# Optimization experiments

Measured on AMD Instinct MI355X. Metric: run time of the kernel, lower is better.

Reference implementation:

```python
import jax, jax.numpy as jnp
import numpy as np

N, E, B, IN, H = 20000, 50000, 1024, 32, 64

def setup_inputs() -> dict:
    key = jax.random.key(0)
    ks = jax.random.split(key, 32)
    d = {}
    d["x"] = jax.random.normal(ks[0], (N, IN), jnp.float32)
    d["edge_index"] = jax.random.randint(ks[1], (2, E), 0, N)
    d["edge_attr"] = jax.random.uniform(ks[2], (E, 6), dtype=jnp.float32)
    d["batch"] = jnp.sort(jax.random.randint(ks[3], (N,), 0, B))
    d["t"] = jax.random.uniform(ks[4], (B, 1), dtype=jnp.float32)
    d["p"] = jax.random.uniform(ks[5], (B, 1), dtype=jnp.float32)
    d["num_graphs"] = B
    def lin(k, fan_in, shape):
        return jax.random.normal(k, shape, jnp.float32) * (1.0 / np.sqrt(fan_in))
    # lin0: IN -> H
    d["W0"] = lin(ks[6], IN, (IN, H)); d["b0"] = jnp.zeros((H,), jnp.float32)
    # edge MLP: 6 -> 64 -> H*H
    d["We1"] = lin(ks[7], 6, (6, 64)); d["be1"] = jnp.zeros((64,), jnp.float32)
    d["We2"] = lin(ks[8], 64, (64, H * H)); d["be2"] = jnp.zeros((H * H,), jnp.float32)
    # NNConv root weight + bias
    d["Wroot"] = lin(ks[9], H, (H, H)); d["bconv"] = jnp.zeros((H,), jnp.float32)
    # GRU (input H, hidden H), torch layout [3H, *] gate order r,z,n
    d["gru_wih"] = lin(ks[10], H, (3 * H, H)); d["gru_whh"] = lin(ks[11], H, (3 * H, H))
    d["gru_bih"] = jnp.zeros((3 * H,), jnp.float32); d["gru_bhh"] = jnp.zeros((3 * H,), jnp.float32)
    # Set2Set LSTM (input 2H, hidden H), torch layout [4H, *] gate order i,f,g,o
    d["l_wih"] = lin(ks[12], 2 * H, (4 * H, 2 * H)); d["l_whh"] = lin(ks[13], H, (4 * H, H))
    d["l_bih"] = jnp.zeros((4 * H,), jnp.float32); d["l_bhh"] = jnp.zeros((4 * H,), jnp.float32)
    # readout MLP
    d["W1"] = lin(ks[14], 2 * H + 2, (2 * H + 2, H)); d["b1"] = jnp.zeros((H,), jnp.float32)
    d["W2"] = lin(ks[15], H, (H, 64)); d["b2"] = jnp.zeros((64,), jnp.float32)
    d["W3"] = lin(ks[16], 64, (64, 1)); d["b3"] = jnp.zeros((1,), jnp.float32)
    return d


def reference(x, edge_attr, t, p, W0, b0, We1, be1, We2, be2, Wroot, bconv,
              gru_wih, gru_whh, gru_bih, gru_bhh, l_wih, l_whh, l_bih, l_bhh,
              W1, b1, W2, b2, W3, b3, edge_index, batch, num_graphs):
    n_nodes = x.shape[0]
    hdim = W0.shape[1]
    src, dst = edge_index[0], edge_index[1]

    out = jax.nn.relu(x @ W0 + b0)            # [N,H]
    h = out

    # edge MLP -> per-edge weight matrices [E,H,H] (edge_attr is loop-invariant)
    ew = (jax.nn.relu(edge_attr @ We1 + be1) @ We2 + be2).reshape(-1, hdim, hdim)

    for _ in range(4):
        # NNConv: gather source features, per-edge matmul, scatter-add to targets
        msg = jnp.einsum('eh,eho->eo', out[src], ew)                 # [E,H]
        agg = jax.ops.segment_sum(msg, dst, num_segments=n_nodes)    # [N,H]
        m = jax.nn.relu(agg + out @ Wroot + bconv)
        # GRU step (single timestep)
        gi = m @ gru_wih.T + gru_bih
        gh = h @ gru_whh.T + gru_bhh
        ir, iz, inn = jnp.split(gi, 3, axis=-1)
        hr, hz, hn = jnp.split(gh, 3, axis=-1)
        r = jax.nn.sigmoid(ir + hr)
        z = jax.nn.sigmoid(iz + hz)
        nn_ = jnp.tanh(inn + r * hn)
        h = (1.0 - z) * nn_ + z * h
        out = h

    # Set2Set pooling, 3 processing steps
    qh = jnp.zeros((num_graphs, hdim), x.dtype)
    qc = jnp.zeros((num_graphs, hdim), x.dtype)
    q_star = jnp.zeros((num_graphs, 2 * hdim), x.dtype)
    for _ in range(3):
        g = q_star @ l_wih.T + l_bih + qh @ l_whh.T + l_bhh
        gi_, gf_, gg_, go_ = jnp.split(g, 4, axis=-1)
        qc = jax.nn.sigmoid(gf_) * qc + jax.nn.sigmoid(gi_) * jnp.tanh(gg_)
        qh = jax.nn.sigmoid(go_) * jnp.tanh(qc)
        q = qh                                                        # [B,H]
        e = jnp.sum(out * q[batch], axis=-1, keepdims=True)          # [N,1]
        emax = jax.ops.segment_max(e, batch, num_segments=num_graphs)
        a = jnp.exp(e - emax[batch])
        asum = jax.ops.segment_sum(a, batch, num_segments=num_graphs)
        a = a / asum[batch]                                           # segment softmax
        r_ = jax.ops.segment_sum(a * out, batch, num_segments=num_graphs)
        q_star = jnp.concatenate([q, r_], axis=-1)

    feat = jnp.concatenate([q_star, t, p], axis=-1)                   # [B,2H+2]
    y = jax.nn.relu(feat @ W1 + b1)
    y = jax.nn.relu(y @ W2 + b2)
    y = y @ W3 + b3
    return y.reshape(-1)
```

## Files before the change

### kernel.cpp

```cpp
#include <hip/hip_runtime.h>
#include <math.h>

#define N_NODES 20000
#define N_EDGES 50000
#define NB      1024
#define IND     32
#define HDIM    64

typedef __attribute__((ext_vector_type(8))) short bf16x8;
typedef __attribute__((ext_vector_type(4))) float f32x4;

static inline size_t align_up(size_t x, size_t a) { return (x + a - 1) & ~(a - 1); }

__device__ __forceinline__ float sigmoidf_(float x) {
    return 1.0f / (1.0f + __expf(-x));
}
__device__ __forceinline__ float tanhf_(float x) {
    float xc = fminf(fmaxf(x, -15.0f), 15.0f);
    float e = __expf(2.0f * xc);
    return (e - 1.0f) / (e + 1.0f);
}
__device__ __forceinline__ unsigned pk2(float p0, float p1) {
    unsigned u0 = __float_as_uint(p0) + 0x8000u;
    unsigned u1 = __float_as_uint(p1) + 0x8000u;
    return __builtin_amdgcn_perm(u1, u0, 0x07060302u);
}
__device__ __forceinline__ unsigned bf1(float v) {
    return (__float_as_uint(v) + 0x8000u) >> 16;
}

__global__ void k_prep(const float* __restrict__ We2, const float* __restrict__ be2,
                       short* __restrict__ We2b,
                       const float* __restrict__ Wroot, const float* __restrict__ gwhh,
                       const float* __restrict__ gwih,
                       short* __restrict__ WB1h, short* __restrict__ WB1l,
                       short* __restrict__ WB2h, short* __restrict__ WB2l,
                       const float* __restrict__ lwih, const float* __restrict__ lwhh,
                       float* __restrict__ lwihP, float* __restrict__ lwhhP,
                       const int* __restrict__ batch, int* __restrict__ offs) {
    int bid = blockIdx.x, tid = threadIdx.x;
    if (bid < 1040) {
        int idx = bid * 256 + tid;
        int s = idx >> 12;
        int col = idx & 4095;
        int k = col >> 6, o = col & 63;
        float val = (s < 64) ? We2[k * 4096 + s * 64 + o] : be2[k * 64 + o];
        int dst = s * 4096 + (((o >> 4) * 128 + (k >> 5) * 64 + ((k >> 3) & 3) * 16 + (o & 15)) << 3) + (k & 7);
        We2b[dst] = (short)bf1(val);
    } else if (bid < 1152) {
        int idx = (bid - 1040) * 256 + tid;
        if (idx < 28672) {
            bool b1 = idx < 16384;
            int li = b1 ? idx : idx - 16384;
            int j = li & 7, lane = (li >> 3) & 63, c = (li >> 9) & 1, otile = li >> 10;
            int k = c * 32 + (lane >> 4) * 8 + j;
            int o = otile * 16 + (lane & 15);
            float val;
            if (b1) val = (o < 64) ? Wroot[k * 64 + o] : gwhh[(o - 64) * 64 + k];
            else    val = gwih[o * 64 + k];
            unsigned hs = bf1(val);
            float lo = val - __uint_as_float(hs << 16);
            unsigned ls = bf1(lo);
            if (b1) { WB1h[li] = (short)hs; WB1l[li] = (short)ls; }
            else    { WB2h[li] = (short)hs; WB2l[li] = (short)ls; }
        }
    } else if (bid < 1280) {
        int idx = (bid - 1152) * 256 + tid;
        int g = idx & 3, j = (idx >> 2) & 63, i = idx >> 8;
        lwihP[idx] = lwih[(g * 64 + j) * 128 + i];
    } else if (bid < 1344) {
        int idx = (bid - 1280) * 256 + tid;
        int g = idx & 3, j = (idx >> 2) & 63, i = idx >> 8;
        lwhhP[idx] = lwhh[(g * 64 + j) * 64 + i];
    } else {
        int i = (bid - 1344) * 256 + tid;
        if (i <= NB) {
            int lo = 0, hi = N_NODES;
            while (lo < hi) { int mid = (lo + hi) >> 1; if (batch[mid] < i) lo = mid + 1; else hi = mid; }
            offs[i] = lo;
        }
    }
}

__global__ void k_count(const int* __restrict__ ei, int* __restrict__ deg) {
    int e = blockIdx.x * 256 + threadIdx.x;
    if (e < N_EDGES) atomicAdd(&deg[ei[N_EDGES + e]], 1);
}

__global__ void k_scan(const int* __restrict__ deg, int* __restrict__ rowptr, int* __restrict__ cursor) {
    __shared__ int s_w[16];
    int t = threadIdx.x;
    int base = t * 20;
    int v[20]; int s = 0;
#pragma unroll
    for (int i = 0; i < 20; ++i) {
        int idx = base + i;
        v[i] = (idx < N_NODES) ? deg[idx] : 0;
        s += v[i];
    }
    int lane = t & 63, w = t >> 6;
    int inc = s;
#pragma unroll
    for (int off = 1; off < 64; off <<= 1) {
        int o = __shfl_up(inc, off);
        if (lane >= off) inc += o;
    }
    if (lane == 63) s_w[w] = inc;
    __syncthreads();
    if (w == 0 && lane < 16) {
        int x = s_w[lane];
        int xs = x;
#pragma unroll
        for (int off = 1; off < 16; off <<= 1) {
            int o = __shfl_up(xs, off);
            if (lane >= off) xs += o;
        }
        s_w[lane] = xs - x;
    }
    __syncthreads();
    int run = s_w[w] + (inc - s);
#pragma unroll
    for (int i = 0; i < 20; ++i) {
        int idx = base + i;
        if (idx < N_NODES) { rowptr[idx] = run; cursor[idx] = run; }
        else if (idx == N_NODES) rowptr[idx] = run;
        run += v[i];
    }
}

__global__ void k_fill(const int* __restrict__ ei, int* __restrict__ cursor, int* __restrict__ perm) {
    int e = blockIdx.x * 256 + threadIdx.x;
    if (e < N_EDGES) {
        int pos = atomicAdd(&cursor[ei[N_EDGES + e]], 1);
        perm[pos] = e;
    }
}

__global__ void k_init_feat(const float* __restrict__ x, const float* __restrict__ W0,
                            const float* __restrict__ b0, float* __restrict__ hbuf,
                            const float* __restrict__ ea, const float* __restrict__ We1,
                            const float* __restrict__ be1, float* __restrict__ re) {
    int bid = blockIdx.x;
    int tid = threadIdx.x;
    int w = tid >> 6, j = tid & 63;
    if (bid < 5000) {
        int n = bid * 4 + w;
        float acc = b0[j];
        const float* xr = x + n * IND;
#pragma unroll
        for (int i = 0; i < IND; ++i) acc = fmaf(xr[i], W0[i * 64 + j], acc);
        hbuf[n * 64 + j] = fmaxf(acc, 0.0f);
    } else {
        int e = (bid - 5000) * 4 + w;
        if (e >= N_EDGES) return;
        float acc = be1[j];
        const float* er = ea + e * 6;
#pragma unroll
        for (int i = 0; i < 6; ++i) acc = fmaf(er[i], We1[i * 64 + j], acc);
        re[e * 64 + j] = fmaxf(acc, 0.0f);
    }
}

__launch_bounds__(256, 3)
__global__ void k_msg_mfma(const float* __restrict__ hbuf, const float* __restrict__ reb,
                           const short* __restrict__ We2b, const int* __restrict__ ei,
                           float* __restrict__ msg) {
    __shared__ float s_v[64][64];
    int tid = threadIdx.x;
    int eb = blockIdx.x * 64;
    int lane = tid & 63;
    int w = tid >> 6;
    int l15 = lane & 15, lhi = lane >> 4;

    {
        int se = tid >> 2;
        int sh = tid & 3;
        int ge = eb + se;
        const float* rowp = (ge < N_EDGES) ? (hbuf + (size_t)ei[ge] * 64) : (const float*)0;
#pragma unroll
        for (int rr4 = 0; rr4 < 4; ++rr4) {
            int hb = rr4 * 16 + sh * 4;
            float4 vv = rowp ? *(const float4*)(rowp + hb) : make_float4(0.f, 0.f, 0.f, 0.f);
            s_v[hb + 0][se] = vv.x; s_v[hb + 1][se] = vv.y;
            s_v[hb + 2][se] = vv.z; s_v[hb + 3][se] = vv.w;
        }
    }

    union U { int4 i4; bf16x8 v; };
    U a_re[4][2];
#pragma unroll
    for (int m = 0; m < 4; ++m) {
        int ge = eb + m * 16 + l15;
        if (ge < N_EDGES) {
            const float* rp = reb + (size_t)ge * 64 + lhi * 8;
            float4 x0 = *(const float4*)(rp);
            float4 x1 = *(const float4*)(rp + 4);
            float4 y0 = *(const float4*)(rp + 32);
            float4 y1 = *(const float4*)(rp + 36);
            a_re[m][0].i4 = make_int4(pk2(x0.x, x0.y), pk2(x0.z, x0.w), pk2(x1.x, x1.y), pk2(x1.z, x1.w));
            a_re[m][1].i4 = make_int4(pk2(y0.x, y0.y), pk2(y0.z, y0.w), pk2(y1.x, y1.y), pk2(y1.z, y1.w));
        } else {
            a_re[m][0].i4 = make_int4(0, 0, 0, 0);
            a_re[m][1].i4 = make_int4(0, 0, 0, 0);
        }
    }

    const int4* bp0 = (const int4*)We2b + (w * 128 + lane);
    const int4* bp1 = bp0 + 64;
    int4 Sc0[4], Sc1[4];
#pragma unroll
    for (int j = 0; j < 4; ++j) {
        Sc0[j] = bp0[j * 512];
        Sc1[j] = bp1[j * 512];
    }

    __syncthreads();

    const f32x4 zero4 = {0.f, 0.f, 0.f, 0.f};
    f32x4 macc[4];
#pragma unroll
    for (int m = 0; m < 4; ++m) macc[m] = zero4;

    float4 vv[4], vn[4];
#pragma unroll
    for (int m = 0; m < 4; ++m) vv[m] = *(const float4*)&s_v[0][m * 16 + lhi * 4];

    for (int g = 0; g < 16; ++g) {
#pragma unroll
        for (int j = 0; j < 4; ++j) {
            int s = g * 4 + j;
            int snext = (s < 63) ? (s + 1) : 63;
#pragma unroll
            for (int m = 0; m < 4; ++m)
                vn[m] = *(const float4*)&s_v[snext][m * 16 + lhi * 4];
            U bb0, bb1; bb0.i4 = Sc0[j]; bb1.i4 = Sc1[j];
#pragma unroll
            for (int m = 0; m < 4; ++m) {
                f32x4 t = __builtin_amdgcn_mfma_f32_16x16x32_bf16(a_re[m][0].v, bb0.v, zero4, 0, 0, 0);
                t = __builtin_amdgcn_mfma_f32_16x16x32_bf16(a_re[m][1].v, bb1.v, t, 0, 0, 0);
                macc[m][0] = fmaf(vv[m].x, t[0], macc[m][0]);
                macc[m][1] = fmaf(vv[m].y, t[1], macc[m][1]);
                macc[m][2] = fmaf(vv[m].z, t[2], macc[m][2]);
                macc[m][3] = fmaf(vv[m].w, t[3], macc[m][3]);
            }
            int sload = (s + 4 <= 64) ? (s + 4) : 64;
            Sc0[j] = bp0[sload * 512];
            Sc1[j] = bp1[sload * 512];
#pragma unroll
            for (int m = 0; m < 4; ++m) vv[m] = vn[m];
        }
    }

    {
        U bb0, bb1; bb0.i4 = Sc0[0]; bb1.i4 = Sc1[0];
#pragma unroll
        for (int m = 0; m < 4; ++m) {
            int e = m * 16 + l15;
            U a0, a1;
            a0.i4 = make_int4(
                pk2(s_v[lhi * 8 + 0][e], s_v[lhi * 8 + 1][e]),
                pk2(s_v[lhi * 8 + 2][e], s_v[lhi * 8 + 3][e]),
                pk2(s_v[lhi * 8 + 4][e], s_v[lhi * 8 + 5][e]),
                pk2(s_v[lhi * 8 + 6][e], s_v[lhi * 8 + 7][e]));
            a1.i4 = make_int4(
                pk2(s_v[32 + lhi * 8 + 0][e], s_v[32 + lhi * 8 + 1][e]),
                pk2(s_v[32 + lhi * 8 + 2][e], s_v[32 + lhi * 8 + 3][e]),
                pk2(s_v[32 + lhi * 8 + 4][e], s_v[32 + lhi * 8 + 5][e]),
                pk2(s_v[32 + lhi * 8 + 6][e], s_v[32 + lhi * 8 + 7][e]));
            macc[m] = __builtin_amdgcn_mfma_f32_16x16x32_bf16(a0.v, bb0.v, macc[m], 0, 0, 0);
            macc[m] = __builtin_amdgcn_mfma_f32_16x16x32_bf16(a1.v, bb1.v, macc[m], 0, 0, 0);
        }
    }
    int o = w * 16 + l15;
#pragma unroll
    for (int m = 0; m < 4; ++m) {
#pragma unroll
        for (int r = 0; r < 4; ++r) {
            int el = m * 16 + lhi * 4 + r;
            int ge = eb + el;
            if (ge < N_EDGES) msg[(size_t)ge * 64 + o] = macc[m][r];
        }
    }
}

__launch_bounds__(256, 4)
__global__ void k_node_update(float* __restrict__ hbuf, const float* __restrict__ msg,
                              const int* __restrict__ rowptr, const int* __restrict__ perm,
                              const short* __restrict__ WB1h, const short* __restrict__ WB1l,
                              const short* __restrict__ WB2h, const short* __restrict__ WB2l,
                              const float* __restrict__ bconv, const float* __restrict__ bih,
                              const float* __restrict__ bhh) {
    __shared__ short s_hh[32][72];
    __shared__ short s_hl[32][72];
    __shared__ short s_mh[32][72];
    __shared__ short s_ml[32][72];
    __shared__ float s_agg[32][68];
    int tid = threadIdx.x;
    int nbase = blockIdx.x * 32;
    int lane = tid & 63, w = tid >> 6;
    int l15 = lane & 15, lhi = lane >> 4;

    {
        int nt = tid >> 3, q = tid & 7;
        int n = nbase + nt;
#pragma unroll
        for (int c4 = 0; c4 < 2; ++c4) {
            int col = q * 8 + c4 * 4;
            float4 v = *(const float4*)&hbuf[(size_t)n * 64 + col];
            unsigned h01 = pk2(v.x, v.y), h23 = pk2(v.z, v.w);
            float f0 = __uint_as_float(h01 << 16);
            float f1 = __uint_as_float(h01 & 0xffff0000u);
            float f2 = __uint_as_float(h23 << 16);
            float f3 = __uint_as_float(h23 & 0xffff0000u);
            unsigned l01 = pk2(v.x - f0, v.y - f1), l23 = pk2(v.z - f2, v.w - f3);
            *(unsigned*)&s_hh[nt][col]     = h01;
            *(unsigned*)&s_hh[nt][col + 2] = h23;
            *(unsigned*)&s_hl[nt][col]     = l01;
            *(unsigned*)&s_hl[nt][col + 2] = l23;
        }
        float4 aggv[2];
#pragma unroll
        for (int c4 = 0; c4 < 2; ++c4)
            aggv[c4] = *(const float4*)&bconv[q * 8 + c4 * 4];
        int rs = rowptr[n], rend = rowptr[n + 1];
        for (int qq = rs; qq < rend; ++qq) {
            const float* mrow = msg + (size_t)perm[qq] * 64 + q * 8;
#pragma unroll
            for (int c4 = 0; c4 < 2; ++c4) {
                float4 mv = *(const float4*)&mrow[c4 * 4];
                aggv[c4].x += mv.x; aggv[c4].y += mv.y;
                aggv[c4].z += mv.z; aggv[c4].w += mv.w;
            }
        }
#pragma unroll
        for (int c4 = 0; c4 < 2; ++c4)
            *(float4*)&s_agg[nt][q * 8 + c4 * 4] = aggv[c4];
    }
    __syncthreads();

    union U { int4 i4; bf16x8 v; };
    U ah[2][2], al[2][2];
#pragma unroll
    for (int m = 0; m < 2; ++m)
#pragma unroll
        for (int c = 0; c < 2; ++c) {
            ah[m][c].i4 = *(const int4*)&s_hh[m * 16 + l15][c * 32 + lhi * 8];
            al[m][c].i4 = *(const int4*)&s_hl[m * 16 + l15][c * 32 + lhi * 8];
        }

    const int4* B1h = (const int4*)WB1h;
    const int4* B1l = (const int4*)WB1l;
    const int4* B2h = (const int4*)WB2h;
    const int4* B2l = (const int4*)WB2l;

    f32x4 C0[2], G[3][2], I[3][2];

    {
        int ot = w;
        U bh0, bh1, bl0, bl1;
        bh0.i4 = B1h[(ot * 2 + 0) * 64 + lane];
        bh1.i4 = B1h[(ot * 2 + 1) * 64 + lane];
        bl0.i4 = B1l[(ot * 2 + 0) * 64 + lane];
        bl1.i4 = B1l[(ot * 2 + 1) * 64 + lane];
#pragma unroll
        for (int m = 0; m < 2; ++m) {
            f32x4 c;
#pragma unroll
            for (int r = 0; r < 4; ++r) c[r] = s_agg[m * 16 + lhi * 4 + r][w * 16 + l15];
            c = __builtin_amdgcn_mfma_f32_16x16x32_bf16(ah[m][0].v, bh0.v, c, 0, 0, 0);
            c = __builtin_amdgcn_mfma_f32_16x16x32_bf16(ah[m][1].v, bh1.v, c, 0, 0, 0);
            c = __builtin_amdgcn_mfma_f32_16x16x32_bf16(al[m][0].v, bh0.v, c, 0, 0, 0);
            c = __builtin_amdgcn_mfma_f32_16x16x32_bf16(al[m][1].v, bh1.v, c, 0, 0, 0);
            c = __builtin_amdgcn_mfma_f32_16x16x32_bf16(ah[m][0].v, bl0.v, c, 0, 0, 0);
            c = __builtin_amdgcn_mfma_f32_16x16x32_bf16(ah[m][1].v, bl1.v, c, 0, 0, 0);
            C0[m] = c;
        }
    }
#pragma unroll
    for (int m = 0; m < 2; ++m)
#pragma unroll
        for (int r = 0; r < 4; ++r) {
            float mv = fmaxf(C0[m][r], 0.0f);
            int row = m * 16 + lhi * 4 + r, col = w * 16 + l15;
            unsigned hs = bf1(mv);
            float lof = mv - __uint_as_float(hs << 16);
            s_mh[row][col] = (short)hs;
            s_ml[row][col] = (short)bf1(lof);
        }
#pragma unroll
    for (int p = 1; p < 4; ++p) {
        int ot = p * 4 + w;
        U bh0, bh1, bl0, bl1;
        bh0.i4 = B1h[(ot * 2 + 0) * 64 + lane];
        bh1.i4 = B1h[(ot * 2 + 1) * 64 + lane];
        bl0.i4 = B1l[(ot * 2 + 0) * 64 + lane];
        bl1.i4 = B1l[(ot * 2 + 1) * 64 + lane];
        float bv = bhh[(p - 1) * 64 + w * 16 + l15];
#pragma unroll
        for (int m = 0; m < 2; ++m) {
            f32x4 c = {bv, bv, bv, bv};
            c = __builtin_amdgcn_mfma_f32_16x16x32_bf16(ah[m][0].v, bh0.v, c, 0, 0, 0);
            c = __builtin_amdgcn_mfma_f32_16x16x32_bf16(ah[m][1].v, bh1.v, c, 0, 0, 0);
            c = __builtin_amdgcn_mfma_f32_16x16x32_bf16(al[m][0].v, bh0.v, c, 0, 0, 0);
            c = __builtin_amdgcn_mfma_f32_16x16x32_bf16(al[m][1].v, bh1.v, c, 0, 0, 0);
            c = __builtin_amdgcn_mfma_f32_16x16x32_bf16(ah[m][0].v, bl0.v, c, 0, 0, 0);
            c = __builtin_amdgcn_mfma_f32_16x16x32_bf16(ah[m][1].v, bl1.v, c, 0, 0, 0);
            G[p - 1][m] = c;
        }
    }
    __syncthreads();
    U mh[2][2], ml[2][2];
#pragma unroll
    for (int m = 0; m < 2; ++m)
#pragma unroll
        for (int c = 0; c < 2; ++c) {
            mh[m][c].i4 = *(const int4*)&s_mh[m * 16 + l15][c * 32 + lhi * 8];
            ml[m][c].i4 = *(const int4*)&s_ml[m * 16 + l15][c * 32 + lhi * 8];
        }
#pragma unroll
    for (int p = 0; p < 3; ++p) {
        int ot = p * 4 + w;
        U bh0, bh1, bl0, bl1;
        bh0.i4 = B2h[(ot * 2 + 0) * 64 + lane];
        bh1.i4 = B2h[(ot * 2 + 1) * 64 + lane];
        bl0.i4 = B2l[(ot * 2 + 0) * 64 + lane];
        bl1.i4 = B2l[(ot * 2 + 1) * 64 + lane];
        float bv = bih[p * 64 + w * 16 + l15];
#pragma unroll
        for (int m = 0; m < 2; ++m) {
            f32x4 c = {bv, bv, bv, bv};
            c = __builtin_amdgcn_mfma_f32_16x16x32_bf16(mh[m][0].v, bh0.v, c, 0, 0, 0);
            c = __builtin_amdgcn_mfma_f32_16x16x32_bf16(mh[m][1].v, bh1.v, c, 0, 0, 0);
            c = __builtin_amdgcn_mfma_f32_16x16x32_bf16(ml[m][0].v, bh0.v, c, 0, 0, 0);
            c = __builtin_amdgcn_mfma_f32_16x16x32_bf16(ml[m][1].v, bh1.v, c, 0, 0, 0);
            c = __builtin_amdgcn_mfma_f32_16x16x32_bf16(mh[m][0].v, bl0.v, c, 0, 0, 0);
            c = __builtin_amdgcn_mfma_f32_16x16x32_bf16(mh[m][1].v, bl1.v, c, 0, 0, 0);
            I[p][m] = c;
        }
    }
#pragma unroll
    for (int m = 0; m < 2; ++m)
#pragma unroll
        for (int r = 0; r < 4; ++r) {
            int row = m * 16 + lhi * 4 + r;
            int n = nbase + row;
            int col = w * 16 + l15;
            float hold = __uint_as_float(((unsigned)(unsigned short)s_hh[row][col]) << 16)
                       + __uint_as_float(((unsigned)(unsigned short)s_hl[row][col]) << 16);
            float rg = sigmoidf_(I[0][m][r] + G[0][m][r]);
            float z  = sigmoidf_(I[1][m][r] + G[1][m][r]);
            float nn = tanhf_(I[2][m][r] + rg * G[2][m][r]);
            hbuf[(size_t)n * 64 + col] = (1.0f - z) * nn + z * hold;
        }
}

__launch_bounds__(64)
__global__ void k_set2set(const float* __restrict__ hbuf, const int* __restrict__ offs,
                          const float* __restrict__ t, const float* __restrict__ p,
                          const float* __restrict__ lwihP, const float* __restrict__ lwhhP,
                          const float* __restrict__ l_bih, const float* __restrict__ l_bhh,
                          const float* __restrict__ W1, const float* __restrict__ b1,
                          const float* __restrict__ W2, const float* __restrict__ b2,
                          const float* __restrict__ W3, const float* __restrict__ b3,
                          float* __restrict__ y) {
    __shared__ float s_qs[192];
    __shared__ float s_y[64];
    int b = blockIdx.x;
    int j = threadIdx.x;
    int s = offs[b], e = offs[b + 1];
    float qh = 0.f, qc = 0.f, qs0 = 0.f, qs1 = 0.f;
    float bi0 = l_bih[j]       + l_bhh[j];
    float bi1 = l_bih[64 + j]  + l_bhh[64 + j];
    float bi2 = l_bih[128 + j] + l_bhh[128 + j];
    float bi3 = l_bih[192 + j] + l_bhh[192 + j];

    for (int iter = 0; iter < 3; ++iter) {
        s_qs[j] = qs0; s_qs[64 + j] = qs1; s_qs[128 + j] = qh;
        __syncthreads();
        float g0 = bi0, g1 = bi1, g2 = bi2, g3 = bi3;
#pragma unroll 8
        for (int i = 0; i < 128; ++i) {
            float qsv = s_qs[i];
            float4 wv = *(const float4*)&lwihP[(i * 64 + j) * 4];
            g0 = fmaf(qsv, wv.x, g0);
            g1 = fmaf(qsv, wv.y, g1);
            g2 = fmaf(qsv, wv.z, g2);
            g3 = fmaf(qsv, wv.w, g3);
        }
#pragma unroll 8
        for (int i = 0; i < 64; ++i) {
            float qhv = s_qs[128 + i];
            float4 wv = *(const float4*)&lwhhP[(i * 64 + j) * 4];
            g0 = fmaf(qhv, wv.x, g0);
            g1 = fmaf(qhv, wv.y, g1);
            g2 = fmaf(qhv, wv.z, g2);
            g3 = fmaf(qhv, wv.w, g3);
        }
        __syncthreads();
        float ci = sigmoidf_(g0), cf = sigmoidf_(g1);
        float cg = tanhf_(g2),   co = sigmoidf_(g3);
        qc = cf * qc + ci * cg;
        qh = co * tanhf_(qc);
        float qv = qh;
        float mx = -1e30f, l = 0.0f, racc = 0.0f;
        for (int n = s; n < e; ++n) {
            float xv = hbuf[(size_t)n * 64 + j];
            float prod = xv * qv;
#pragma unroll
            for (int off = 32; off > 0; off >>= 1) prod += __shfl_xor(prod, off);
            float mnew = fmaxf(mx, prod);
            float scale = __expf(mx - mnew);
            float wgt = __expf(prod - mnew);
            l = l * scale + wgt;
            racc = racc * scale + wgt * xv;
            mx = mnew;
        }
        float r = (e > s) ? (racc / l) : 0.0f;
        qs0 = qv; qs1 = r;
    }
    s_qs[j] = qs0; s_qs[64 + j] = qs1;
    __syncthreads();
    float acc = b1[j];
#pragma unroll 8
    for (int i = 0; i < 128; ++i) acc = fmaf(s_qs[i], W1[i * 64 + j], acc);
    acc = fmaf(t[b], W1[128 * 64 + j], acc);
    acc = fmaf(p[b], W1[129 * 64 + j], acc);
    acc = fmaxf(acc, 0.0f);
    s_y[j] = acc;
    __syncthreads();
    float acc2 = b2[j];
#pragma unroll 8
    for (int i = 0; i < 64; ++i) acc2 = fmaf(s_y[i], W2[i * 64 + j], acc2);
    acc2 = fmaxf(acc2, 0.0f);
    float part = acc2 * W3[j];
#pragma unroll
    for (int off = 32; off > 0; off >>= 1) part += __shfl_xor(part, off);
    if (j == 0) y[b] = part + b3[0];
}

extern "C" void kernel_launch(void* const* d_in, const int* in_sizes, int n_in,
                              void* d_out, int out_size, void* d_ws, size_t ws_size,
                              hipStream_t stream) {
    const float* x     = (const float*)d_in[0];
    const int*   ei    = (const int*)  d_in[1];
    const float* ea    = (const float*)d_in[2];
    const int*   batch = (const int*)  d_in[3];
    const float* t     = (const float*)d_in[4];
    const float* p     = (const float*)d_in[5];
    const float* W0    = (const float*)d_in[7];
    const float* b0    = (const float*)d_in[8];
    const float* We1   = (const float*)d_in[9];
    const float* be1   = (const float*)d_in[10];
    const float* We2   = (const float*)d_in[11];
    const float* be2   = (const float*)d_in[12];
    const float* Wroot = (const float*)d_in[13];
    const float* bconv = (const float*)d_in[14];
    const float* gwih  = (const float*)d_in[15];
    const float* gwhh  = (const float*)d_in[16];
    const float* gbih  = (const float*)d_in[17];
    const float* gbhh  = (const float*)d_in[18];
    const float* lwih  = (const float*)d_in[19];
    const float* lwhh  = (const float*)d_in[20];
    const float* lbih  = (const float*)d_in[21];
    const float* lbhh  = (const float*)d_in[22];
    const float* W1    = (const float*)d_in[23];
    const float* b1    = (const float*)d_in[24];
    const float* W2    = (const float*)d_in[25];
    const float* b2    = (const float*)d_in[26];
    const float* W3    = (const float*)d_in[27];
    const float* b3    = (const float*)d_in[28];
    float* y = (float*)d_out;

    char* ws = (char*)d_ws;
    size_t off = 0;
    auto alloc = [&](size_t nbytes) {
        void* ptr = (void*)(ws + off);
        off += align_up(nbytes, 256);
        return ptr;
    };
    float* hbuf   = (float*)alloc((size_t)N_NODES * 64 * 4);
    float* reb    = (float*)alloc((size_t)N_EDGES * 64 * 4);
    float* msg    = (float*)alloc((size_t)N_EDGES * 64 * 4);
    short* We2b   = (short*)alloc((size_t)65 * 4096 * 2);
    short* WB1h   = (short*)alloc(16384 * 2);
    short* WB1l   = (short*)alloc(16384 * 2);
    short* WB2h   = (short*)alloc(12288 * 2);
    short* WB2l   = (short*)alloc(12288 * 2);
    float* lwihP  = (float*)alloc(32768 * 4);
    float* lwhhP  = (float*)alloc(16384 * 4);
    int*   offs   = (int*)  alloc((NB + 1) * 4);
    int*   deg    = (int*)  alloc(N_NODES * 4);
    int*   rowptr = (int*)  alloc((N_NODES + 1) * 4);
    int*   cursor = (int*)  alloc(N_NODES * 4);
    int*   perm   = (int*)  alloc(N_EDGES * 4);

    k_prep<<<1349, 256, 0, stream>>>(We2, be2, We2b, Wroot, gwhh, gwih,
                                     WB1h, WB1l, WB2h, WB2l,
                                     lwih, lwhh, lwihP, lwhhP, batch, offs);
    hipMemsetAsync(deg, 0, (size_t)N_NODES * 4, stream);
    k_count<<<(N_EDGES + 255) / 256, 256, 0, stream>>>(ei, deg);
    k_scan<<<1, 1024, 0, stream>>>(deg, rowptr, cursor);
    k_fill<<<(N_EDGES + 255) / 256, 256, 0, stream>>>(ei, cursor, perm);

    k_init_feat<<<17500, 256, 0, stream>>>(x, W0, b0, hbuf, ea, We1, be1, reb);

    for (int it = 0; it < 4; ++it) {
        k_msg_mfma<<<(N_EDGES + 63) / 64, 256, 0, stream>>>(hbuf, reb, We2b, ei, msg);
        k_node_update<<<N_NODES / 32, 256, 0, stream>>>(hbuf, msg, rowptr, perm,
                                                        WB1h, WB1l, WB2h, WB2l,
                                                        bconv, gbih, gbhh);
    }

    k_set2set<<<NB, 64, 0, stream>>>(hbuf, offs, t, p, lwihP, lwhhP, lbih, lbhh,
                                     W1, b1, W2, b2, W3, b3, y);
}
```

Measured before the change: 446.7 us.

## Widen Set2Set blocks to four waves, splitting gate rows and node softmax

The Set2Set kernel now runs 256 threads per graph instead of 64. Each thread computes one LSTM gate pre-activation using transposed weights, and the four waves each take every fourth node in the online softmax. The partial max, sum and accumulator values are then merged in shared memory. This exposes more parallelism for the serial per-graph loop, at the cost of extra barriers and a cross-wave merge step.

```diff
diff --git a/kernel.cpp b/kernel.cpp
--- a/kernel.cpp
+++ b/kernel.cpp
@@ -36,7 +36,7 @@
                        short* __restrict__ WB1h, short* __restrict__ WB1l,
                        short* __restrict__ WB2h, short* __restrict__ WB2l,
                        const float* __restrict__ lwih, const float* __restrict__ lwhh,
-                       float* __restrict__ lwihP, float* __restrict__ lwhhP,
+                       float* __restrict__ lwihT, float* __restrict__ lwhhT,
                        const int* __restrict__ batch, int* __restrict__ offs) {
     int bid = blockIdx.x, tid = threadIdx.x;
     if (bid < 1040) {
@@ -66,12 +66,12 @@
         }
     } else if (bid < 1280) {
         int idx = (bid - 1152) * 256 + tid;
-        int g = idx & 3, j = (idx >> 2) & 63, i = idx >> 8;
-        lwihP[idx] = lwih[(g * 64 + j) * 128 + i];
+        int i = idx >> 8, j = idx & 255;
+        lwihT[idx] = lwih[j * 128 + i];
     } else if (bid < 1344) {
         int idx = (bid - 1280) * 256 + tid;
-        int g = idx & 3, j = (idx >> 2) & 63, i = idx >> 8;
-        lwhhP[idx] = lwhh[(g * 64 + j) * 64 + i];
+        int i = idx >> 8, j = idx & 255;
+        lwhhT[idx] = lwhh[j * 64 + i];
     } else {
         int i = (bid - 1344) * 256 + tid;
         if (i <= NB) {
@@ -454,57 +454,53 @@
         }
 }
 
-__launch_bounds__(64)
+__launch_bounds__(256)
 __global__ void k_set2set(const float* __restrict__ hbuf, const int* __restrict__ offs,
                           const float* __restrict__ t, const float* __restrict__ p,
-                          const float* __restrict__ lwihP, const float* __restrict__ lwhhP,
+                          const float* __restrict__ lwihT, const float* __restrict__ lwhhT,
                           const float* __restrict__ l_bih, const float* __restrict__ l_bhh,
                           const float* __restrict__ W1, const float* __restrict__ b1,
                           const float* __restrict__ W2, const float* __restrict__ b2,
                           const float* __restrict__ W3, const float* __restrict__ b3,
                           float* __restrict__ y) {
     __shared__ float s_qs[192];
+    __shared__ float s_g[256];
+    __shared__ float s_racc[4][64];
+    __shared__ float s_m[4], s_l[4];
     __shared__ float s_y[64];
     int b = blockIdx.x;
-    int j = threadIdx.x;
+    int tid = threadIdx.x;
+    int w = tid >> 6, lane = tid & 63;
     int s = offs[b], e = offs[b + 1];
-    float qh = 0.f, qc = 0.f, qs0 = 0.f, qs1 = 0.f;
-    float bi0 = l_bih[j]       + l_bhh[j];
-    float bi1 = l_bih[64 + j]  + l_bhh[64 + j];
-    float bi2 = l_bih[128 + j] + l_bhh[128 + j];
-    float bi3 = l_bih[192 + j] + l_bhh[192 + j];
+    float bi = l_bih[tid] + l_bhh[tid];
+    float qc = 0.f;
+
+    if (tid < 192) s_qs[tid] = 0.f;
+    __syncthreads();
 
     for (int iter = 0; iter < 3; ++iter) {
-        s_qs[j] = qs0; s_qs[64 + j] = qs1; s_qs[128 + j] = qh;
+        float g = bi;
+#pragma unroll 8
+        for (int i = 0; i < 128; ++i) g = fmaf(s_qs[i], lwihT[i * 256 + tid], g);
+#pragma unroll 8
+        for (int i = 0; i < 64; ++i)  g = fmaf(s_qs[128 + i], lwhhT[i * 256 + tid], g);
+        s_g[tid] = g;
         __syncthreads();
-        float g0 = bi0, g1 = bi1, g2 = bi2, g3 = bi3;
-#pragma unroll 8
-        for (int i = 0; i < 128; ++i) {
-            float qsv = s_qs[i];
-            float4 wv = *(const float4*)&lwihP[(i * 64 + j) * 4];
-            g0 = fmaf(qsv, wv.x, g0);
-            g1 = fmaf(qsv, wv.y, g1);
-            g2 = fmaf(qsv, wv.z, g2);
-            g3 = fmaf(qsv, wv.w, g3);
-        }
-#pragma unroll 8
-        for (int i = 0; i < 64; ++i) {
-            float qhv = s_qs[128 + i];
-            float4 wv = *(const float4*)&lwhhP[(i * 64 + j) * 4];
-            g0 = fmaf(qhv, wv.x, g0);
-            g1 = fmaf(qhv, wv.y, g1);
-            g2 = fmaf(qhv, wv.z, g2);
-            g3 = fmaf(qhv, wv.w, g3);
+        if (w == 0) {
+            float ci = sigmoidf_(s_g[lane]);
+            float cf = sigmoidf_(s_g[64 + lane]);
+            float cg = tanhf_(s_g[128 + lane]);
+            float co = sigmoidf_(s_g[192 + lane]);
+            qc = cf * qc + ci * cg;
+            float qh = co * tanhf_(qc);
+            s_qs[lane] = qh;
+            s_qs[128 + lane] = qh;
         }
         __syncthreads();
-        float ci = sigmoidf_(g0), cf = sigmoidf_(g1);
-        float cg = tanhf_(g2),   co = sigmoidf_(g3);
-        qc = cf * qc + ci * cg;
-        qh = co * tanhf_(qc);
-        float qv = qh;
+        float qv = s_qs[128 + lane];
         float mx = -1e30f, l = 0.0f, racc = 0.0f;
-        for (int n = s; n < e; ++n) {
-            float xv = hbuf[(size_t)n * 64 + j];
+        for (int n = s + w; n < e; n += 4) {
+            float xv = hbuf[(size_t)n * 64 + lane];
             float prod = xv * qv;
 #pragma unroll
             for (int off = 32; off > 0; off >>= 1) prod += __shfl_xor(prod, off);
@@ -515,27 +511,39 @@
             racc = racc * scale + wgt * xv;
             mx = mnew;
         }
-        float r = (e > s) ? (racc / l) : 0.0f;
-        qs0 = qv; qs1 = r;
-    }
-    s_qs[j] = qs0; s_qs[64 + j] = qs1;
-    __syncthreads();
-    float acc = b1[j];
+        s_racc[w][lane] = racc;
+        if (lane == 0) { s_m[w] = mx; s_l[w] = l; }
+        __syncthreads();
+        if (w == 0) {
+            float M = fmaxf(fmaxf(s_m[0], s_m[1]), fmaxf(s_m[2], s_m[3]));
+            float L = 0.f, R = 0.f;
+#pragma unroll
+            for (int ww = 0; ww < 4; ++ww) {
+                float sc = __expf(s_m[ww] - M);
+                L += s_l[ww] * sc;
+                R = fmaf(s_racc[ww][lane], sc, R);
+            }
+            s_qs[64 + lane] = (e > s) ? (R / L) : 0.0f;
+        }
+        __syncthreads();
+    }
+    if (w == 0) {
+        float acc = b1[lane];
 #pragma unroll 8
-    for (int i = 0; i < 128; ++i) acc = fmaf(s_qs[i], W1[i * 64 + j], acc);
-    acc = fmaf(t[b], W1[128 * 64 + j], acc);
-    acc = fmaf(p[b], W1[129 * 64 + j], acc);
-    acc = fmaxf(acc, 0.0f);
-    s_y[j] = acc;
-    __syncthreads();
-    float acc2 = b2[j];
+        for (int i = 0; i < 128; ++i) acc = fmaf(s_qs[i], W1[i * 64 + lane], acc);
+        acc = fmaf(t[b], W1[128 * 64 + lane], acc);
+        acc = fmaf(p[b], W1[129 * 64 + lane], acc);
+        acc = fmaxf(acc, 0.0f);
+        s_y[lane] = acc;
+        float acc2 = b2[lane];
 #pragma unroll 8
-    for (int i = 0; i < 64; ++i) acc2 = fmaf(s_y[i], W2[i * 64 + j], acc2);
-    acc2 = fmaxf(acc2, 0.0f);
-    float part = acc2 * W3[j];
-#pragma unroll
-    for (int off = 32; off > 0; off >>= 1) part += __shfl_xor(part, off);
-    if (j == 0) y[b] = part + b3[0];
+        for (int i = 0; i < 64; ++i) acc2 = fmaf(s_y[i], W2[i * 64 + lane], acc2);
+        acc2 = fmaxf(acc2, 0.0f);
+        float part = acc2 * W3[lane];
+#pragma unroll
+        for (int off = 32; off > 0; off >>= 1) part += __shfl_xor(part, off);
+        if (lane == 0) y[b] = part + b3[0];
+    }
 }
 
 extern "C" void kernel_launch(void* const* d_in, const int* in_sizes, int n_in,
@@ -586,8 +594,8 @@
     short* WB1l   = (short*)alloc(16384 * 2);
     short* WB2h   = (short*)alloc(12288 * 2);
     short* WB2l   = (short*)alloc(12288 * 2);
-    float* lwihP  = (float*)alloc(32768 * 4);
-    float* lwhhP  = (float*)alloc(16384 * 4);
+    float* lwihT  = (float*)alloc(32768 * 4);
+    float* lwhhT  = (float*)alloc(16384 * 4);
     int*   offs   = (int*)  alloc((NB + 1) * 4);
     int*   deg    = (int*)  alloc(N_NODES * 4);
     int*   rowptr = (int*)  alloc((N_NODES + 1) * 4);
@@ -596,7 +604,7 @@
 
     k_prep<<<1349, 256, 0, stream>>>(We2, be2, We2b, Wroot, gwhh, gwih,
                                      WB1h, WB1l, WB2h, WB2l,
-                                     lwih, lwhh, lwihP, lwhhP, batch, offs);
+                                     lwih, lwhh, lwihT, lwhhT, batch, offs);
     hipMemsetAsync(deg, 0, (size_t)N_NODES * 4, stream);
     k_count<<<(N_EDGES + 255) / 256, 256, 0, stream>>>(ei, deg);
     k_scan<<<1, 1024, 0, stream>>>(deg, rowptr, cursor);
@@ -611,6 +619,6 @@
                                                         bconv, gbih, gbhh);
     }
 
-    k_set2set<<<NB, 64, 0, stream>>>(hbuf, offs, t, p, lwihP, lwhhP, lbih, lbhh,
-                                     W1, b1, W2, b2, W3, b3, y);
-}
+    k_set2set<<<NB, 256, 0, stream>>>(hbuf, offs, t, p, lwihT, lwhhT, lbih, lbhh,
+                                      W1, b1, W2, b2, W3, b3, y);
+}
```

Measured after the change: 414.1 us. 1.08x faster.
